# Optimization experiments

Hardware: AMD Instinct MI355X
Metric: run time of the kernel (lower is better)

## Reference

```python
import jax, jax.numpy as jnp
import numpy as np

B, S, D_IN, D_H, D_OUT, NB = 4, 4096, 1024, 1024, 1024, 8
BD = D_H // NB  # block size of the block-diagonal gate projections
R_MIN, R_MAX, EPS = 0.9, 0.999, 1e-8


def setup_inputs() -> dict:
    key = jax.random.key(0)
    ks = jax.random.split(key, 8)
    x = jax.random.normal(ks[0], (B, S, D_IN), dtype=jnp.float32)
    h0 = jnp.zeros((B, D_H), dtype=jnp.float32)
    # input projection Dense(d_hidden)
    W_in = jax.random.normal(ks[1], (D_IN, D_H), dtype=jnp.float32) / np.sqrt(D_IN)
    b_in = jnp.zeros((D_H,), dtype=jnp.float32)
    # two BlockDiagonalLinear gate projections (n_blocks blocks of [BD, BD])
    Wgx = jax.random.normal(ks[2], (NB, BD, BD), dtype=jnp.float32) / np.sqrt(BD)
    bgx = jnp.zeros((D_H,), dtype=jnp.float32)
    Wga = jax.random.normal(ks[3], (NB, BD, BD), dtype=jnp.float32) / np.sqrt(BD)
    bga = jnp.zeros((D_H,), dtype=jnp.float32)
    # stable_init_real: softplus(param) == -log(r) with r ~ U[r_min, r_max] in magnitude
    u = jax.random.uniform(ks[4], (D_H,), dtype=jnp.float32)
    a_real = 0.5 * jnp.log(u * (R_MAX**2 - R_MIN**2) + R_MIN**2 + EPS)
    a_real_param = jnp.log(jnp.exp(-a_real) - 1.0)
    # output projection Dense(d_out)
    W_out = jax.random.normal(ks[5], (D_H, D_OUT), dtype=jnp.float32) / np.sqrt(D_H)
    b_out = jnp.zeros((D_OUT,), dtype=jnp.float32)
    return dict(x=x, h0=h0, W_in=W_in, b_in=b_in, Wgx=Wgx, bgx=bgx,
                Wga=Wga, bga=bga, a_real_param=a_real_param,
                W_out=W_out, b_out=b_out)


def _block_diag_linear(x, W, b):
    # x: [B,S,D_H] -> split into NB blocks of BD, per-block matmul
    xb = x.reshape(x.shape[0], x.shape[1], NB, BD)
    y = jnp.einsum('bsni,nio->bsno', xb, W)
    return y.reshape(x.shape[0], x.shape[1], D_H) + b


def reference(x, h0, W_in, b_in, Wgx, bgx, Wga, bga, a_real_param, W_out, b_out):
    # input projection
    x = x @ W_in + b_in  # [B,S,D_H]
    # input-dependent gates (sigmoid of block-diagonal projections)
    gate_x = jax.nn.sigmoid(_block_diag_linear(x, Wgx, bgx))
    gate_a = jax.nn.sigmoid(_block_diag_linear(x, Wga, bga))
    # real-only RG-LRU recurrence coefficient: a = exp(-8 * gate_a * softplus(c))
    log_a = -8.0 * gate_a * jax.nn.softplus(a_real_param)  # [B,S,D_H], <= 0
    a = jnp.exp(log_a)
    # gated input with sqrt(1 - a^2) normalization (sqrt_bound_derivative fwd == sqrt)
    gx = gate_x * x * jnp.sqrt(1.0 - jnp.exp(2.0 * log_a))
    # fold initial state into the first step: h_1 = a_1 * h0 + gx_1
    gx = gx.at[:, 0].add(a[:, 0] * h0)
    # linear scan h_t = a_t * h_{t-1} + gx_t via associative scan over seq axis
    def combine(c1, c2):
        a1, x1 = c1
        a2, x2 = c2
        return (a2 * a1, a2 * x1 + x2)
    _, h = jax.lax.associative_scan(combine, (a, gx), axis=1)  # [B,S,D_H]
    out = h @ W_out + b_out  # [B,S,D_OUT]
    return out, h[:, -1]
```

## Files before the change

### kernel.cpp

```cpp
#include <hip/hip_runtime.h>

#define B_SZ 4
#define SEQ 4096
#define DIN 1024
#define DH 1024
#define DOUT 1024
#define NBLK 8
#define MTOK (B_SZ * SEQ)
#define CHUNK 64
#define NCHUNK (SEQ / CHUNK)

typedef _Float16 half8 __attribute__((ext_vector_type(8)));
typedef _Float16 half4v __attribute__((ext_vector_type(4)));
typedef float f32x4 __attribute__((ext_vector_type(4)));

__device__ __forceinline__ void gl_lds16(const void* g, void* l) {
  __builtin_amdgcn_global_load_lds((__attribute__((address_space(1))) void*)g,
                                   (__attribute__((address_space(3))) void*)l,
                                   16, 0, 0);
}

__device__ __forceinline__ int swz_h(int r, int c) {
  return (((r << 8) | (c << 1)) ^ ((r & 7) << 4)) >> 1;
}

__global__ __launch_bounds__(256)
void prep_kernel(const float* __restrict__ x, _Float16* __restrict__ x_h,
                 const float* __restrict__ Win, const float* __restrict__ Wout,
                 const float* __restrict__ Wgx, const float* __restrict__ Wga,
                 _Float16* __restrict__ WinT, _Float16* __restrict__ WoutT,
                 _Float16* __restrict__ WgxT, _Float16* __restrict__ WgaT) {
  __shared__ float tile[64][65];
  if (blockIdx.x < 16384) {
    const int gid = blockIdx.x * 256 + threadIdx.x;
    const float4 v = ((const float4*)x)[gid];
    half4v h;
    h[0] = (_Float16)v.x; h[1] = (_Float16)v.y; h[2] = (_Float16)v.z; h[3] = (_Float16)v.w;
    ((half4v*)x_h)[gid] = h;
    return;
  }
  int t = blockIdx.x - 16384;
  const float* src; _Float16* dst; int C; size_t bo = 0;
  if (t < 256)      { src = Win;  dst = WinT;  C = 1024; }
  else if (t < 512) { src = Wout; dst = WoutT; C = 1024; t -= 256; }
  else if (t < 544) { int u = t - 512; src = Wgx; dst = WgxT; C = 128;
                      bo = (size_t)(u >> 2) * (128 * 128); t = u & 3; }
  else              { int u = t - 544; src = Wga; dst = WgaT; C = 128;
                      bo = (size_t)(u >> 2) * (128 * 128); t = u & 3; }
  const int nbx = C >> 6;
  const int r0 = (t / nbx) * 64, c0 = (t % nbx) * 64;
  const int tr = threadIdx.x >> 6, tc = threadIdx.x & 63;
#pragma unroll
  for (int i = 0; i < 64; i += 4)
    tile[tr + i][tc] = src[bo + (size_t)(r0 + tr + i) * C + c0 + tc];
  __syncthreads();
#pragma unroll
  for (int i = 0; i < 64; i += 4) {
    const int cc = i + tr;
    dst[bo + (size_t)(c0 + cc) * C + r0 + tc] = (_Float16)tile[tc][cc];
  }
}

template <int OUT_F32>
__global__ __launch_bounds__(256)
void gemm_bt(const _Float16* __restrict__ A, const _Float16* __restrict__ Bt,
             const float* __restrict__ bias, void* __restrict__ C,
             int M, int N, int K) {
  __shared__ __align__(16) _Float16 As[128 * 64];
  __shared__ __align__(16) _Float16 Bs[128 * 64];
  const int tid = threadIdx.x;
  const int wave = tid >> 6, lane = tid & 63;
  const int m0 = blockIdx.x * 128, n0 = blockIdx.y * 128;
  const int wm = (wave >> 1) * 64, wn = (wave & 1) * 64;
  const int row = lane & 15, quad = lane >> 4;
  const int srow = lane >> 3, scol = (lane & 7) * 8;

  f32x4 acc[4][4] = {};
  for (int kt = 0; kt < K; kt += 64) {
#pragma unroll
    for (int ci = 0; ci < 4; ci++) {
      const int c = wave * 4 + ci;
      gl_lds16(A  + (size_t)(m0 + c * 8 + srow) * K + kt + scol, As + c * 512);
      gl_lds16(Bt + (size_t)(n0 + c * 8 + srow) * K + kt + scol, Bs + c * 512);
    }
    __syncthreads();
#pragma unroll
    for (int kk = 0; kk < 64; kk += 32) {
      half8 af[4], bf[4];
#pragma unroll
      for (int i = 0; i < 4; i++)
        af[i] = *(const half8*)&As[(wm + i * 16 + row) * 64 + kk + quad * 8];
#pragma unroll
      for (int i = 0; i < 4; i++)
        bf[i] = *(const half8*)&Bs[(wn + i * 16 + row) * 64 + kk + quad * 8];
#pragma unroll
      for (int i = 0; i < 4; i++)
#pragma unroll
        for (int j = 0; j < 4; j++)
          acc[i][j] = __builtin_amdgcn_mfma_f32_16x16x32_f16(af[i], bf[j], acc[i][j], 0, 0, 0);
    }
    __syncthreads();
  }
  float bv[4];
#pragma unroll
  for (int j = 0; j < 4; j++) bv[j] = bias[n0 + wn + j * 16 + row];
#pragma unroll
  for (int i = 0; i < 4; i++) {
#pragma unroll
    for (int r = 0; r < 4; r++) {
      const int m = m0 + wm + i * 16 + quad * 4 + r;
      const size_t base = (size_t)m * N + n0 + wn + row;
#pragma unroll
      for (int j = 0; j < 4; j++) {
        const float v = acc[i][j][r] + bv[j];
        if (OUT_F32) ((float*)C)[base + j * 16] = v;
        else         ((_Float16*)C)[base + j * 16] = (_Float16)v;
      }
    }
  }
}

__global__ __launch_bounds__(256)
void gemm1_gates(const _Float16* __restrict__ A, const _Float16* __restrict__ Bt,
                 const float* __restrict__ bias,
                 const _Float16* __restrict__ WxT, const _Float16* __restrict__ WaT,
                 const float* __restrict__ bgx, const float* __restrict__ bga,
                 const float* __restrict__ arp,
                 _Float16* __restrict__ a_out, _Float16* __restrict__ gx_out,
                 float* __restrict__ cA, float* __restrict__ cH) {
  __shared__ __align__(16) _Float16 smem[128 * 128];
  _Float16* const As = smem;
  _Float16* const Bs = smem + 128 * 64;
  const int tid = threadIdx.x;
  const int wave = tid >> 6, lane = tid & 63;
  const int m0 = blockIdx.x * 128, nb = blockIdx.y, n0 = nb * 128;
  const int wm = (wave >> 1) * 64, wn = (wave & 1) * 64;
  const int row = lane & 15, quad = lane >> 4;
  const int srow = lane >> 3, scol = (lane & 7) * 8;

  f32x4 acc[4][4] = {};
  for (int kt = 0; kt < DIN; kt += 64) {
#pragma unroll
    for (int ci = 0; ci < 4; ci++) {
      const int c = wave * 4 + ci;
      gl_lds16(A  + (size_t)(m0 + c * 8 + srow) * DIN + kt + scol, As + c * 512);
      gl_lds16(Bt + (size_t)(n0 + c * 8 + srow) * DIN + kt + scol, Bs + c * 512);
    }
    __syncthreads();
#pragma unroll
    for (int kk = 0; kk < 64; kk += 32) {
      half8 af[4], bf[4];
#pragma unroll
      for (int i = 0; i < 4; i++)
        af[i] = *(const half8*)&As[(wm + i * 16 + row) * 64 + kk + quad * 8];
#pragma unroll
      for (int i = 0; i < 4; i++)
        bf[i] = *(const half8*)&Bs[(wn + i * 16 + row) * 64 + kk + quad * 8];
#pragma unroll
      for (int i = 0; i < 4; i++)
#pragma unroll
        for (int j = 0; j < 4; j++)
          acc[i][j] = __builtin_amdgcn_mfma_f32_16x16x32_f16(af[i], bf[j], acc[i][j], 0, 0, 0);
    }
    __syncthreads();
  }

  {
    float bv[4];
#pragma unroll
    for (int j = 0; j < 4; j++) bv[j] = bias[n0 + wn + j * 16 + row];
#pragma unroll
    for (int i = 0; i < 4; i++)
#pragma unroll
      for (int r = 0; r < 4; r++) {
        const int tl = wm + i * 16 + quad * 4 + r;
#pragma unroll
        for (int j = 0; j < 4; j++)
          smem[swz_h(tl, wn + j * 16 + row)] = (_Float16)(acc[i][j][r] + bv[j]);
      }
  }
  __syncthreads();

  const _Float16* const WxB = WxT + (size_t)nb * (128 * 128);
  const _Float16* const WaB = WaT + (size_t)nb * (128 * 128);
  const int b_idx = (m0 + wm) >> 12;
  const int c_idx = ((m0 + wm) & (SEQ - 1)) >> 6;
  const int cbase = c_idx * (B_SZ * DH) + b_idx * DH + n0 + wn + row;

#pragma unroll 1
  for (int jp = 0; jp < 2; jp++) {
    f32x4 accx[4][2] = {}, acca[4][2] = {};
#pragma unroll
    for (int kk = 0; kk < 128; kk += 32) {
      half8 af[4];
#pragma unroll
      for (int i = 0; i < 4; i++)
        af[i] = *(const half8*)&smem[swz_h(wm + i * 16 + row, kk + quad * 8)];
#pragma unroll
      for (int jj = 0; jj < 2; jj++) {
        const size_t wo = (size_t)(wn + (jp * 2 + jj) * 16 + row) * 128 + kk + quad * 8;
        const half8 bx = *(const half8*)&WxB[wo];
        const half8 ba = *(const half8*)&WaB[wo];
#pragma unroll
        for (int i = 0; i < 4; i++) {
          accx[i][jj] = __builtin_amdgcn_mfma_f32_16x16x32_f16(af[i], bx, accx[i][jj], 0, 0, 0);
          acca[i][jj] = __builtin_amdgcn_mfma_f32_16x16x32_f16(af[i], ba, acca[i][jj], 0, 0, 0);
        }
      }
    }
    float bxv[2], bav[2], cd[2];
#pragma unroll
    for (int jj = 0; jj < 2; jj++) {
      const int d = n0 + wn + (jp * 2 + jj) * 16 + row;
      bxv[jj] = bgx[d]; bav[jj] = bga[d];
      cd[jj] = log1pf(expf(arp[d]));
    }
    float Arun[2] = {1.f, 1.f}, Hrun[2] = {0.f, 0.f};
#pragma unroll
    for (int i = 0; i < 4; i++) {
      float Aseg[2] = {1.f, 1.f}, Hseg[2] = {0.f, 0.f};
#pragma unroll
      for (int r = 0; r < 4; r++) {
        const int tl = wm + i * 16 + quad * 4 + r;
        const size_t rowbase = (size_t)(m0 + tl) * DH + n0 + wn + row;
        _Float16 ah[2], gh[2];
#pragma unroll
        for (int jj = 0; jj < 2; jj++) {
          const float px = accx[i][jj][r] + bxv[jj];
          const float pa = acca[i][jj][r] + bav[jj];
          const float sx = 1.f / (1.f + __expf(-px));
          const float sa = 1.f / (1.f + __expf(-pa));
          const float a = __expf(-8.f * sa * cd[jj]);
          const float n2 = fmaxf(1.f - a * a, 0.f);
          const float xv = (float)smem[swz_h(tl, wn + (jp * 2 + jj) * 16 + row)];
          ah[jj] = (_Float16)a;
          gh[jj] = (_Float16)(sx * xv * sqrtf(n2));
          const float ar = (float)ah[jj], gr = (float)gh[jj];
          Aseg[jj] *= ar;
          Hseg[jj] = fmaf(ar, Hseg[jj], gr);
        }
#pragma unroll
        for (int jj = 0; jj < 2; jj++) a_out[rowbase + (jp * 2 + jj) * 16] = ah[jj];
#pragma unroll
        for (int jj = 0; jj < 2; jj++) gx_out[rowbase + (jp * 2 + jj) * 16] = gh[jj];
      }
#pragma unroll
      for (int jj = 0; jj < 2; jj++) {
        float A1 = Aseg[jj], H1 = Hseg[jj];
        float A2 = __shfl_down(A1, 16, 64), H2 = __shfl_down(H1, 16, 64);
        H1 = fmaf(A2, H1, H2); A1 *= A2;
        A2 = __shfl_down(A1, 32, 64); H2 = __shfl_down(H1, 32, 64);
        H1 = fmaf(A2, H1, H2); A1 *= A2;
        Hrun[jj] = fmaf(A1, Hrun[jj], H1);
        Arun[jj] *= A1;
      }
    }
    if (lane < 16) {
#pragma unroll
      for (int jj = 0; jj < 2; jj++) {
        cA[cbase + (jp * 2 + jj) * 16] = Arun[jj];
        cH[cbase + (jp * 2 + jj) * 16] = Hrun[jj];
      }
    }
  }
}

__global__ __launch_bounds__(256)
void scan_p2(const float* __restrict__ cA, const float* __restrict__ cH,
             const float* __restrict__ h0, float* __restrict__ cin,
             float* __restrict__ hlast) {
  const int wave = threadIdx.x >> 6, lane = threadIdx.x & 63;
  const int g = blockIdx.x * 4 + wave;
  float A = cA[(size_t)lane * (B_SZ * DH) + g], H = cH[(size_t)lane * (B_SZ * DH) + g];
#pragma unroll
  for (int d = 1; d < 64; d <<= 1) {
    const float Ap = __shfl_up(A, d, 64), Hp = __shfl_up(H, d, 64);
    if (lane >= d) { H = fmaf(A, Hp, H); A *= Ap; }
  }
  const float h0g = h0[g];
  if (lane == 63) hlast[g] = fmaf(A, h0g, H);
  float Ae = __shfl_up(A, 1, 64), He = __shfl_up(H, 1, 64);
  if (lane == 0) { Ae = 1.f; He = 0.f; }
  cin[(size_t)lane * (B_SZ * DH) + g] = fmaf(Ae, h0g, He);
}

__global__ __launch_bounds__(256)
void scan_p3(const _Float16* __restrict__ a, const _Float16* __restrict__ gx,
             const float* __restrict__ cin, _Float16* __restrict__ h) {
  const int gtid = blockIdx.x * 256 + threadIdx.x;
  const int d = gtid & (DH - 1);
  const int bc = gtid >> 10;
  const int b = bc >> 6, c = bc & (NCHUNK - 1);
  const size_t base = ((size_t)(b * SEQ + c * CHUNK)) * DH + d;
  float carry = cin[c * (B_SZ * DH) + b * DH + d];
#pragma unroll 4
  for (int i = 0; i < CHUNK; i++) {
    const float av = (float)a[base + (size_t)i * DH];
    const float gv = (float)gx[base + (size_t)i * DH];
    carry = fmaf(av, carry, gv);
    h[base + (size_t)i * DH] = (_Float16)carry;
  }
}

extern "C" void kernel_launch(void* const* d_in, const int* in_sizes, int n_in,
                              void* d_out, int out_size, void* d_ws, size_t ws_size,
                              hipStream_t stream) {
  const float* x     = (const float*)d_in[0];
  const float* h0    = (const float*)d_in[1];
  const float* W_in  = (const float*)d_in[2];
  const float* b_in  = (const float*)d_in[3];
  const float* Wgx   = (const float*)d_in[4];
  const float* bgx   = (const float*)d_in[5];
  const float* Wga   = (const float*)d_in[6];
  const float* bga   = (const float*)d_in[7];
  const float* arp   = (const float*)d_in[8];
  const float* W_out = (const float*)d_in[9];
  const float* b_out = (const float*)d_in[10];
  float* out = (float*)d_out;
  float* hlast = out + (size_t)MTOK * DOUT;

  char* p = (char*)d_ws;
  auto take = [&](size_t bytes) { char* r = p; p += (bytes + 255) & ~(size_t)255; return r; };
  _Float16* x_h   = (_Float16*)take((size_t)MTOK * DIN * 2);
  _Float16* a_buf = (_Float16*)take((size_t)MTOK * DH * 2);
  _Float16* gxb   = (_Float16*)take((size_t)MTOK * DH * 2);
  _Float16* WinT  = (_Float16*)take((size_t)DIN * DH * 2);
  _Float16* WoutT = (_Float16*)take((size_t)DH * DOUT * 2);
  _Float16* WgxT  = (_Float16*)take((size_t)NBLK * 128 * 128 * 2);
  _Float16* WgaT  = (_Float16*)take((size_t)NBLK * 128 * 128 * 2);
  float* cA   = (float*)take((size_t)NCHUNK * B_SZ * DH * 4);
  float* cH   = (float*)take((size_t)NCHUNK * B_SZ * DH * 4);
  float* cin  = (float*)take((size_t)NCHUNK * B_SZ * DH * 4);
  _Float16* h_buf = x_h;

  prep_kernel<<<16384 + 576, 256, 0, stream>>>(x, x_h, W_in, W_out, Wgx, Wga,
                                               WinT, WoutT, WgxT, WgaT);
  gemm1_gates<<<dim3(MTOK / 128, NBLK), 256, 0, stream>>>(
      x_h, WinT, b_in, WgxT, WgaT, bgx, bga, arp, a_buf, gxb, cA, cH);
  scan_p2<<<(B_SZ * DH) / 4, 256, 0, stream>>>(cA, cH, h0, cin, hlast);
  scan_p3<<<(B_SZ * NCHUNK * DH) / 256, 256, 0, stream>>>(a_buf, gxb, cin, h_buf);
  gemm_bt<1><<<dim3(MTOK / 128, DOUT / 128), 256, 0, stream>>>(h_buf, WoutT, b_out, out, MTOK, DOUT, DH);
}
```

Before: 374.9 us.

## Pack a and gx into interleaved MFMA-fragment layout for coalesced stores

The gate kernel now packs the fp16 a and gx values into one 32-bit word and writes them in the MFMA fragment order, so each wave's stores are contiguous 64-lane dwords instead of scattered 2-byte stores across rows. The scan kernel reads that layout with remapped indexing. It also adds an occupancy hint of 4 blocks per CU and stops the K loop from unrolling. The cost is that the scan reads become more strided in the fragment layout, and register limits may rise under the launch bound.

```diff
diff --git a/kernel.cpp b/kernel.cpp
--- a/kernel.cpp
+++ b/kernel.cpp
@@ -13,6 +13,8 @@
 typedef _Float16 half8 __attribute__((ext_vector_type(8)));
 typedef _Float16 half4v __attribute__((ext_vector_type(4)));
 typedef float f32x4 __attribute__((ext_vector_type(4)));
+
+union HPack { unsigned int u; _Float16 h[2]; };
 
 __device__ __forceinline__ void gl_lds16(const void* g, void* l) {
   __builtin_amdgcn_global_load_lds((__attribute__((address_space(1))) void*)g,
@@ -120,13 +122,13 @@
   }
 }
 
-__global__ __launch_bounds__(256)
+__global__ __launch_bounds__(256, 4)
 void gemm1_gates(const _Float16* __restrict__ A, const _Float16* __restrict__ Bt,
                  const float* __restrict__ bias,
                  const _Float16* __restrict__ WxT, const _Float16* __restrict__ WaT,
                  const float* __restrict__ bgx, const float* __restrict__ bga,
                  const float* __restrict__ arp,
-                 _Float16* __restrict__ a_out, _Float16* __restrict__ gx_out,
+                 unsigned int* __restrict__ ag,
                  float* __restrict__ cA, float* __restrict__ cH) {
   __shared__ __align__(16) _Float16 smem[128 * 128];
   _Float16* const As = smem;
@@ -139,6 +141,7 @@
   const int srow = lane >> 3, scol = (lane & 7) * 8;
 
   f32x4 acc[4][4] = {};
+#pragma unroll 1
   for (int kt = 0; kt < DIN; kt += 64) {
 #pragma unroll
     for (int ci = 0; ci < 4; ci++) {
@@ -186,6 +189,7 @@
   const int b_idx = (m0 + wm) >> 12;
   const int c_idx = ((m0 + wm) & (SEQ - 1)) >> 6;
   const int cbase = c_idx * (B_SZ * DH) + b_idx * DH + n0 + wn + row;
+  const size_t agbase = ((size_t)(blockIdx.x * NBLK + nb) * 4 + wave) * 4096;
 
 #pragma unroll 1
   for (int jp = 0; jp < 2; jp++) {
@@ -222,8 +226,6 @@
 #pragma unroll
       for (int r = 0; r < 4; r++) {
         const int tl = wm + i * 16 + quad * 4 + r;
-        const size_t rowbase = (size_t)(m0 + tl) * DH + n0 + wn + row;
-        _Float16 ah[2], gh[2];
 #pragma unroll
         for (int jj = 0; jj < 2; jj++) {
           const float px = accx[i][jj][r] + bxv[jj];
@@ -233,16 +235,14 @@
           const float a = __expf(-8.f * sa * cd[jj]);
           const float n2 = fmaxf(1.f - a * a, 0.f);
           const float xv = (float)smem[swz_h(tl, wn + (jp * 2 + jj) * 16 + row)];
-          ah[jj] = (_Float16)a;
-          gh[jj] = (_Float16)(sx * xv * sqrtf(n2));
-          const float ar = (float)ah[jj], gr = (float)gh[jj];
+          HPack pk;
+          pk.h[0] = (_Float16)a;
+          pk.h[1] = (_Float16)(sx * xv * sqrtf(n2));
+          ag[agbase + (size_t)(((i * 4 + r) * 4) + jp * 2 + jj) * 64 + lane] = pk.u;
+          const float ar = (float)pk.h[0], gr = (float)pk.h[1];
           Aseg[jj] *= ar;
           Hseg[jj] = fmaf(ar, Hseg[jj], gr);
         }
-#pragma unroll
-        for (int jj = 0; jj < 2; jj++) a_out[rowbase + (jp * 2 + jj) * 16] = ah[jj];
-#pragma unroll
-        for (int jj = 0; jj < 2; jj++) gx_out[rowbase + (jp * 2 + jj) * 16] = gh[jj];
       }
 #pragma unroll
       for (int jj = 0; jj < 2; jj++) {
@@ -285,20 +285,26 @@
 }
 
 __global__ __launch_bounds__(256)
-void scan_p3(const _Float16* __restrict__ a, const _Float16* __restrict__ gx,
+void scan_p3(const unsigned int* __restrict__ ag,
              const float* __restrict__ cin, _Float16* __restrict__ h) {
   const int gtid = blockIdx.x * 256 + threadIdx.x;
   const int d = gtid & (DH - 1);
   const int bc = gtid >> 10;
   const int b = bc >> 6, c = bc & (NCHUNK - 1);
-  const size_t base = ((size_t)(b * SEQ + c * CHUNK)) * DH + d;
+  const int mblk = b * 32 + (c >> 1), wmb = c & 1;
+  const int nb = d >> 7, wnb = (d >> 6) & 1, j = (d >> 4) & 3, row = d & 15;
+  const size_t agb = ((size_t)(mblk * NBLK + nb) * 4 + wmb * 2 + wnb) * 4096
+                   + j * 64 + row;
+  const size_t hbase = ((size_t)(b * SEQ + c * CHUNK)) * DH + d;
   float carry = cin[c * (B_SZ * DH) + b * DH + d];
 #pragma unroll 4
-  for (int i = 0; i < CHUNK; i++) {
-    const float av = (float)a[base + (size_t)i * DH];
-    const float gv = (float)gx[base + (size_t)i * DH];
+  for (int t = 0; t < CHUNK; t++) {
+    HPack pk;
+    pk.u = ag[agb + (size_t)(((t >> 4) * 4 + (t & 3)) * 4) * 64 + ((t >> 2) & 3) * 16];
+    const float av = (float)pk.h[0];
+    const float gv = (float)pk.h[1];
     carry = fmaf(av, carry, gv);
-    h[base + (size_t)i * DH] = (_Float16)carry;
+    h[hbase + (size_t)t * DH] = (_Float16)carry;
   }
 }
 
@@ -322,8 +328,7 @@
   char* p = (char*)d_ws;
   auto take = [&](size_t bytes) { char* r = p; p += (bytes + 255) & ~(size_t)255; return r; };
   _Float16* x_h   = (_Float16*)take((size_t)MTOK * DIN * 2);
-  _Float16* a_buf = (_Float16*)take((size_t)MTOK * DH * 2);
-  _Float16* gxb   = (_Float16*)take((size_t)MTOK * DH * 2);
+  unsigned int* ag = (unsigned int*)take((size_t)MTOK * DH * 4);
   _Float16* WinT  = (_Float16*)take((size_t)DIN * DH * 2);
   _Float16* WoutT = (_Float16*)take((size_t)DH * DOUT * 2);
   _Float16* WgxT  = (_Float16*)take((size_t)NBLK * 128 * 128 * 2);
@@ -336,8 +341,8 @@
   prep_kernel<<<16384 + 576, 256, 0, stream>>>(x, x_h, W_in, W_out, Wgx, Wga,
                                                WinT, WoutT, WgxT, WgaT);
   gemm1_gates<<<dim3(MTOK / 128, NBLK), 256, 0, stream>>>(
-      x_h, WinT, b_in, WgxT, WgaT, bgx, bga, arp, a_buf, gxb, cA, cH);
+      x_h, WinT, b_in, WgxT, WgaT, bgx, bga, arp, ag, cA, cH);
   scan_p2<<<(B_SZ * DH) / 4, 256, 0, stream>>>(cA, cH, h0, cin, hlast);
-  scan_p3<<<(B_SZ * NCHUNK * DH) / 256, 256, 0, stream>>>(a_buf, gxb, cin, h_buf);
+  scan_p3<<<(B_SZ * NCHUNK * DH) / 256, 256, 0, stream>>>(ag, cin, h_buf);
   gemm_bt<1><<<dim3(MTOK / 128, DOUT / 128), 256, 0, stream>>>(h_buf, WoutT, b_out, out, MTOK, DOUT, DH);
 }
```

Result: faster. 314.7 us (-16.1%).
